# Kernel optimization log

Hardware: AMD Instinct MI355X
Metric: run time of the kernel (lower is better)

Reference implementation:

```python
import jax, jax.numpy as jnp
import numpy as np

B, S, E, H = 4, 4096, 1024, 128

def setup_inputs() -> dict:
    key = jax.random.key(0)
    kx, kk, kq, kv = jax.random.split(key, 4)
    x = jax.random.normal(kx, (B, S, E), dtype=jnp.float32)
    # torch nn.Linear weights are [out_features, in_features]
    Wk = jax.random.normal(kk, (H, E), dtype=jnp.float32) * (E ** -0.5)
    Wq = jax.random.normal(kq, (H, E), dtype=jnp.float32) * (E ** -0.5)
    Wv = jax.random.normal(kv, (H, E), dtype=jnp.float32) * (E ** -0.5)
    return {"x": x, "Wk": Wk, "Wq": Wq, "Wv": Wv}

def reference(x, Wk, Wq, Wv):
    # projections: y = x @ W.T  (bias-free nn.Linear)
    k = jnp.einsum('bse,he->bsh', x, Wk)
    q = jnp.einsum('bse,he->bsh', x, Wq)
    v = jnp.einsum('bse,he->bsh', x, Wv)
    emb = x.shape[-1]
    # scores scaled by embedding_size**-0.5 (as in the source, not head_size)
    scores = jnp.einsum('bqh,bkh->bqk', q, k) * (emb ** -0.5)  # [B,S,S]
    # causal mask: positions j > i get -inf
    i = jnp.arange(scores.shape[-2])[:, None]
    j = jnp.arange(scores.shape[-1])[None, :]
    scores = jnp.where(j > i, jnp.float32(-jnp.inf), scores)
    probs = jax.nn.softmax(scores, axis=-1)
    # dropout is identity in eval mode
    out = jnp.einsum('bqk,bkh->bqh', probs, v)  # [B,S,H]
    return out
```

## Files before the change

kernel.cpp:

```cpp
#include <hip/hip_runtime.h>

typedef short bf16x8 __attribute__((ext_vector_type(8)));
typedef float f32x4 __attribute__((ext_vector_type(4)));

#define MFMA16(a, b, c) __builtin_amdgcn_mfma_f32_16x16x32_bf16(a, b, c, 0, 0, 0)

constexpr int Bn = 4, Sn = 4096, En = 1024, Hn = 128;
constexpr float CSCALE = 1.44269504089f * 0.03125f;

__device__ inline int sbase(int qt2) {
    int a = qt2 >> 3, r = qt2 & 7;
    return (a + 1) * (4 * a + r);
}
constexpr int SLOT2_F = 16640;
constexpr int NIT = 320;

__device__ inline unsigned short f2bf(float f) {
    unsigned int u = __builtin_bit_cast(unsigned int, f);
    u += 0x7fff + ((u >> 16) & 1);
    return (unsigned short)(u >> 16);
}

__device__ inline unsigned int pk2(float a, float b) {
    unsigned int ua = __builtin_bit_cast(unsigned int, a) + 0x8000u;
    unsigned int ub = __builtin_bit_cast(unsigned int, b) + 0x8000u;
    return __builtin_amdgcn_perm(ub, ua, 0x07060302u);
}

__device__ inline void gld16(const unsigned short* g, unsigned short* l) {
    __builtin_amdgcn_global_load_lds((const __attribute__((address_space(1))) void*)g,
                                     (__attribute__((address_space(3))) void*)l, 16, 0, 0);
}

__global__ __launch_bounds__(256) void prep_kernel(
    const float* __restrict__ Wk, const float* __restrict__ Wq, const float* __restrict__ Wv,
    unsigned short* __restrict__ wb, unsigned int* __restrict__ sched)
{
    int gy = blockIdx.x >> 5;
    const float* src = (gy == 0) ? Wq : (gy == 1) ? Wk : Wv;
    unsigned short* dst = wb + (size_t)gy * Hn * En;
    int t = (blockIdx.x & 31) * 256 + threadIdx.x;
    const float4* s4 = (const float4*)src;
    for (int i = 0; i < 4; ++i) {
        float4 v = s4[(size_t)t * 4 + i];
        uint2 w2 = { pk2(v.x, v.y), pk2(v.z, v.w) };
        *(uint2*)&dst[(size_t)t * 16 + i * 4] = w2;
    }
    if (blockIdx.x == 0 && threadIdx.x < 80) {
        const int p = threadIdx.x;
        int qt2 = 0, ch = 0, acc = 0;
        for (int q = 0; q < 32; ++q) {
            int n = (q >> 3) + 1;
            if (p < acc + n) { qt2 = q; ch = p - acc; break; }
            acc += n;
        }
        int nloc = min(16, 2 * qt2 + 2 - 16 * ch);
        int key = nloc * 64 + qt2;
        int rank = 0;
        for (int p2 = 0; p2 < 80; ++p2) {
            int q2 = 0, c2 = 0, a2 = 0;
            for (int q = 0; q < 32; ++q) {
                int n = (q >> 3) + 1;
                if (p2 < a2 + n) { q2 = q; c2 = p2 - a2; break; }
                a2 += n;
            }
            int nl2 = min(16, 2 * q2 + 2 - 16 * c2);
            int k2 = nl2 * 64 + q2;
            if (k2 > key || (k2 == key && p2 < p)) ++rank;
        }
        for (int b = 0; b < 4; ++b)
            sched[rank * 4 + b] = (unsigned int)(qt2 | (ch << 6) | (b << 8));
    }
}

__global__ __launch_bounds__(256, 3) void proj_kernel(
    const float* __restrict__ x, const unsigned short* __restrict__ wb,
    unsigned short* __restrict__ qb, unsigned short* __restrict__ kb,
    unsigned short* __restrict__ vbT)
{
    __shared__ __align__(16) unsigned short xs[2][64][64];
    __shared__ __align__(16) unsigned short wsm[2][128][64];

    const int gy = blockIdx.y;
    const unsigned short* wg = wb + (size_t)gy * Hn * En;

    const int m0 = blockIdx.x * 64;
    const int tid = threadIdx.x;
    const int lane = tid & 63, wave = tid >> 6;
    const int l15 = lane & 15, quad = lane >> 4;
    const int wm = (wave & 1) * 32;
    const int wn = (wave >> 1) * 64;

    f32x4 acc[2][4] = {};
    float4 xp[4];

    auto loadx = [&](int kc) {
        for (int p4 = 0; p4 < 4; ++p4) {
            int i = p4 * 256 + tid, row = i >> 4, c4 = (i & 15) * 4;
            xp[p4] = *(const float4*)&x[(size_t)(m0 + row) * En + kc * 64 + c4];
        }
    };
    auto writex = [&](int c) {
        for (int p4 = 0; p4 < 4; ++p4) {
            int i = p4 * 256 + tid, row = i >> 4, hc = i & 15;
            uint2 w2 = { pk2(xp[p4].x, xp[p4].y), pk2(xp[p4].z, xp[p4].w) };
            *(uint2*)((char*)&xs[c][0][0] + row * 128 + (((hc >> 1) ^ (row & 7)) << 4) + ((hc & 1) << 3)) = w2;
        }
    };
    auto issueW = [&](int kc, int c) {
        for (int j = 0; j < 4; ++j) {
            int seg = (wave * 4 + j) * 1024;
            int d = seg + (lane << 4);
            int row = d >> 7, chp = (d >> 4) & 7;
            gld16(wg + (size_t)row * En + kc * 64 + ((chp ^ (row & 7)) << 3),
                  (unsigned short*)((char*)&wsm[c][0][0] + seg));
        }
    };

    loadx(0);
    issueW(0, 0);
    writex(0);
    loadx(1);

    for (int kc = 0; kc < En / 64; ++kc) {
        const int c = kc & 1;
        __syncthreads();
        if (kc + 1 < En / 64) {
            issueW(kc + 1, c ^ 1);
            writex(c ^ 1);
            int kn = (kc + 2 < En / 64) ? kc + 2 : En / 64 - 1;
            loadx(kn);
        }
        bf16x8 xf[2][2], wf[4][2];
        for (int i = 0; i < 2; ++i)
            for (int kk = 0; kk < 2; ++kk) {
                int row = wm + i * 16 + l15;
                int chn = (kk * 4 + quad) ^ (row & 7);
                xf[i][kk] = *(const bf16x8*)((char*)&xs[c][0][0] + row * 128 + (chn << 4));
            }
        for (int j = 0; j < 4; ++j)
            for (int kk = 0; kk < 2; ++kk) {
                int row = wn + j * 16 + l15;
                int chn = (kk * 4 + quad) ^ (row & 7);
                wf[j][kk] = *(const bf16x8*)((char*)&wsm[c][0][0] + row * 128 + (chn << 4));
            }
        if (gy != 2) {
            for (int kk = 0; kk < 2; ++kk)
                for (int i = 0; i < 2; ++i)
                    for (int j = 0; j < 4; ++j)
                        acc[i][j] = MFMA16(xf[i][kk], wf[j][kk], acc[i][j]);
        } else {
            for (int kk = 0; kk < 2; ++kk)
                for (int i = 0; i < 2; ++i)
                    for (int j = 0; j < 4; ++j)
                        acc[i][j] = MFMA16(wf[j][kk], xf[i][kk], acc[i][j]);
        }
    }

    if (gy != 2) {
        unsigned short* ob = (gy == 0) ? qb : kb;
        const float osc = (gy == 0) ? CSCALE : 1.0f;
        for (int i = 0; i < 2; ++i) {
            int rowb = m0 + wm + i * 16 + quad * 4;
            for (int j = 0; j < 4; ++j) {
                int col = wn + j * 16 + l15;
                for (int r = 0; r < 4; ++r)
                    ob[(size_t)(rowb + r) * Hn + col] = f2bf(acc[i][j][r] * osc);
            }
        }
    } else {
        for (int j = 0; j < 4; ++j) {
            int hb = wn + j * 16 + quad * 4;
            for (int i = 0; i < 2; ++i) {
                int sp = m0 + wm + i * 16 + l15;
                int bb = sp >> 12, ss = sp & 4095;
                for (int r = 0; r < 4; ++r)
                    vbT[((size_t)(bb * 128 + hb + r)) * Sn + ss] = f2bf(acc[i][j][r]);
            }
        }
    }
}

__global__ __launch_bounds__(256, 2) void attn_kernel(
    const unsigned short* __restrict__ qb, const unsigned short* __restrict__ kb,
    const unsigned short* __restrict__ vbT, float* __restrict__ out,
    float* __restrict__ part, const unsigned int* __restrict__ sched)
{
    __shared__ unsigned short ks[64][132];
    __shared__ unsigned short vt[128][68];
    __shared__ unsigned short ps[4][32][72];

    const unsigned int wi = sched[blockIdx.x];
    const int qt2 = (int)(wi & 63u);
    const int ch  = (int)((wi >> 6) & 3u);
    const int b   = (int)((wi >> 8) & 3u);
    const int T2  = 2 * qt2 + 2;
    const int nch = (qt2 >> 3) + 1;
    const int t0 = ch * 16;
    const int nloc = min(16, T2 - t0);
    const int q0 = qt2 * 128;

    const int tid = threadIdx.x;
    const int lane = tid & 63, wave = tid >> 6;
    const int l15 = lane & 15, quad = lane >> 4;

    const unsigned short* qg = qb + (size_t)(b * Sn + q0) * Hn;
    bf16x8 qf[2][4];
    for (int g = 0; g < 2; ++g)
        for (int f = 0; f < 4; ++f)
            qf[g][f] = *(const bf16x8*)&qg[(wave * 32 + g * 16 + l15) * Hn + f * 32 + quad * 8];

    f32x4 o[2][8] = {};
    float m_r[2] = { -INFINITY, -INFINITY }, l_r[2] = { 0.f, 0.f };

    const unsigned short* kg = kb + (size_t)b * Sn * Hn;
    const unsigned short* vg = vbT + (size_t)b * 128 * Sn;

    bf16x8 kreg[4], vreg[4];
    auto loadKV = [&](int gt) {
        int kt0 = gt * 64;
        for (int p4 = 0; p4 < 4; ++p4) {
            int i = p4 * 256 + tid;
            kreg[p4] = *(const bf16x8*)&kg[(size_t)(kt0 + (i >> 4)) * Hn + (i & 15) * 8];
            vreg[p4] = *(const bf16x8*)&vg[(size_t)(i >> 3) * Sn + kt0 + (i & 7) * 8];
        }
    };

    loadKV(t0);
    for (int tl = 0; tl < nloc; ++tl) {
        const int gt = t0 + tl;
        for (int p4 = 0; p4 < 4; ++p4) {
            int i = p4 * 256 + tid;
            *(bf16x8*)&ks[i >> 4][(i & 15) * 8] = kreg[p4];
            *(bf16x8*)&vt[i >> 3][(i & 7) * 8] = vreg[p4];
        }
        __syncthreads();
        if (tl + 1 < nloc) loadKV(gt + 1);

        float u[2][4][4];
        for (int nt = 0; nt < 4; ++nt) {
            f32x4 s0 = {}, s1 = {};
            for (int kk = 0; kk < 4; ++kk) {
                bf16x8 kf = *(const bf16x8*)&ks[nt * 16 + l15][kk * 32 + quad * 8];
                s0 = MFMA16(kf, qf[0][kk], s0);
                s1 = MFMA16(kf, qf[1][kk], s1);
            }
            for (int r = 0; r < 4; ++r) { u[0][nt][r] = s0[r]; u[1][nt][r] = s1[r]; }
        }
        if (gt >= 2 * qt2) {
            int kof = (gt - 2 * qt2) * 64;
            for (int g = 0; g < 2; ++g) {
                int qq = wave * 32 + g * 16 + l15;
                for (int nt = 0; nt < 4; ++nt)
                    for (int r = 0; r < 4; ++r)
                        if (kof + nt * 16 + quad * 4 + r > qq) u[g][nt][r] = -INFINITY;
            }
        }
        for (int g = 0; g < 2; ++g) {
            float mx = -INFINITY;
            for (int nt = 0; nt < 4; ++nt)
                for (int r = 0; r < 4; ++r) mx = fmaxf(mx, u[g][nt][r]);
            mx = fmaxf(mx, __shfl_xor(mx, 16));
            mx = fmaxf(mx, __shfl_xor(mx, 32));
            float mn = fmaxf(m_r[g], mx);
            float alpha = exp2f(m_r[g] - mn);
            m_r[g] = mn;
            float sum = 0.f;
            for (int nt = 0; nt < 4; ++nt)
                for (int r = 0; r < 4; ++r) {
                    float pv = exp2f(u[g][nt][r] - mn);
                    u[g][nt][r] = pv;
                    sum += pv;
                }
            sum += __shfl_xor(sum, 16);
            sum += __shfl_xor(sum, 32);
            l_r[g] = l_r[g] * alpha + sum;

            unsigned short* psrow = &ps[wave][g * 16 + l15][0];
            for (int nt = 0; nt < 4; ++nt) {
                uint2 w2 = { pk2(u[g][nt][0], u[g][nt][1]), pk2(u[g][nt][2], u[g][nt][3]) };
                *(uint2*)&psrow[nt * 16 + quad * 4] = w2;
            }
            for (int t = 0; t < 8; ++t) o[g][t] *= alpha;
        }

        for (int k2 = 0; k2 < 2; ++k2) {
            bf16x8 pf0 = *(const bf16x8*)&ps[wave][0 * 16 + l15][k2 * 32 + quad * 8];
            bf16x8 pf1 = *(const bf16x8*)&ps[wave][1 * 16 + l15][k2 * 32 + quad * 8];
            for (int t = 0; t < 8; ++t) {
                bf16x8 vf = *(const bf16x8*)&vt[t * 16 + l15][k2 * 32 + quad * 8];
                o[0][t] = MFMA16(vf, pf0, o[0][t]);
                o[1][t] = MFMA16(vf, pf1, o[1][t]);
            }
        }
        __syncthreads();
    }

    if (nch == 1) {
        for (int g = 0; g < 2; ++g) {
            float inv = 1.0f / l_r[g];
            float* og = out + (size_t)(b * Sn + q0 + wave * 32 + g * 16 + l15) * Hn;
            for (int t = 0; t < 8; ++t) {
                float4 st = { o[g][t][0] * inv, o[g][t][1] * inv, o[g][t][2] * inv, o[g][t][3] * inv };
                *(float4*)&og[t * 16 + quad * 4] = st;
            }
        }
    } else {
        float* P = part + (size_t)(b * 80 + sbase(qt2) + ch) * SLOT2_F;
        for (int g = 0; g < 2; ++g) {
            int q = wave * 32 + g * 16 + l15;
            for (int t = 0; t < 8; ++t) {
                float4 st = { o[g][t][0], o[g][t][1], o[g][t][2], o[g][t][3] };
                *(float4*)&P[q * 128 + t * 16 + quad * 4] = st;
            }
            if (quad == 0) {
                P[16384 + q] = m_r[g];
                P[16512 + q] = l_r[g];
            }
        }
    }
}

__global__ __launch_bounds__(256) void merge_kernel(
    const float* __restrict__ part, float* __restrict__ out)
{
    const int qt2 = 8 + (blockIdx.x >> 1);
    const int half = blockIdx.x & 1;
    const int b = blockIdx.y;
    const int nch = (qt2 >> 3) + 1;
    const float* P0 = part + (size_t)(b * 80 + sbase(qt2)) * SLOT2_F;
    const int q = half * 64 + (threadIdx.x >> 2);
    const int h0 = (threadIdx.x & 3) * 32;

    float m[4], w[4];
    float M = -INFINITY;
    for (int c = 0; c < nch; ++c) {
        m[c] = P0[(size_t)c * SLOT2_F + 16384 + q];
        M = fmaxf(M, m[c]);
    }
    float L = 0.f;
    for (int c = 0; c < nch; ++c) {
        w[c] = exp2f(m[c] - M);
        L += w[c] * P0[(size_t)c * SLOT2_F + 16512 + q];
    }
    float inv = 1.0f / L;

    float acc[32] = {};
    for (int c = 0; c < nch; ++c) {
        const float* Pq = P0 + (size_t)c * SLOT2_F + q * 128 + h0;
        for (int j = 0; j < 8; ++j) {
            float4 v = *(const float4*)&Pq[j * 4];
            acc[j * 4 + 0] += w[c] * v.x;
            acc[j * 4 + 1] += w[c] * v.y;
            acc[j * 4 + 2] += w[c] * v.z;
            acc[j * 4 + 3] += w[c] * v.w;
        }
    }
    float* og = out + (size_t)(b * Sn + qt2 * 128 + q) * Hn + h0;
    for (int j = 0; j < 8; ++j) {
        float4 st = { acc[j * 4 + 0] * inv, acc[j * 4 + 1] * inv,
                      acc[j * 4 + 2] * inv, acc[j * 4 + 3] * inv };
        *(float4*)&og[j * 4] = st;
    }
}

extern "C" void kernel_launch(void* const* d_in, const int* in_sizes, int n_in,
                              void* d_out, int out_size, void* d_ws, size_t ws_size,
                              hipStream_t stream)
{
    const float* x  = (const float*)d_in[0];
    const float* Wk = (const float*)d_in[1];
    const float* Wq = (const float*)d_in[2];
    const float* Wv = (const float*)d_in[3];
    float* out = (float*)d_out;

    unsigned short* qbuf  = (unsigned short*)d_ws;
    unsigned short* kbuf  = qbuf + (size_t)Bn * Sn * Hn;
    unsigned short* vbufT = kbuf + (size_t)Bn * Sn * Hn;
    unsigned short* wb    = vbufT + (size_t)Bn * Sn * Hn;
    float* part = (float*)(wb + (size_t)3 * Hn * En);
    unsigned int* sched = (unsigned int*)part;

    prep_kernel<<<96, 256, 0, stream>>>(Wk, Wq, Wv, wb, sched);
    proj_kernel<<<dim3(Bn * Sn / 64, 3), 256, 0, stream>>>(x, wb, qbuf, kbuf, vbufT);
    attn_kernel<<<NIT, 256, 0, stream>>>(qbuf, kbuf, vbufT, out, part, sched);
    merge_kernel<<<dim3(48, Bn), 256, 0, stream>>>(part, out);
}
```

Measured before the change: 186.8 us.

## Fuse QKV projection into one block, split attention finer, read K/V directly

The projection kernel now computes Q, K and V together in 512-thread blocks, so each x tile is read and converted once instead of three times. V is written transposed with packed 8-byte stores. Attention work is split into 8-tile chunks, and a new schedule places 768 items into 256-slot bins, with empty slots exiting early. The attention kernel drops its LDS staging and barriers for K/V and loads MFMA fragments straight from global memory, relying on cache reuse across waves. This raises occupancy but risks uncoalesced global fragment loads and more partial results to merge.

New measurement: 236.7 us. 1.27x slower.

```diff
diff --git a/kernel.cpp b/kernel.cpp
--- a/kernel.cpp
+++ b/kernel.cpp
@@ -8,12 +8,12 @@
 constexpr int Bn = 4, Sn = 4096, En = 1024, Hn = 128;
 constexpr float CSCALE = 1.44269504089f * 0.03125f;
 
-__device__ inline int sbase(int qt2) {
-    int a = qt2 >> 3, r = qt2 & 7;
-    return (a + 1) * (4 * a + r);
-}
+__device__ inline int sbase2(int qt2) {
+    int g = (qt2 - 4) >> 2, r = (qt2 - 4) & 3;
+    return 2 * g * g + 6 * g + r * (g + 2);
+}
+constexpr int NSLOT = 140;
 constexpr int SLOT2_F = 16640;
-constexpr int NIT = 320;
 
 __device__ inline unsigned short f2bf(float f) {
     unsigned int u = __builtin_bit_cast(unsigned int, f);
@@ -46,73 +46,79 @@
         uint2 w2 = { pk2(v.x, v.y), pk2(v.z, v.w) };
         *(uint2*)&dst[(size_t)t * 16 + i * 4] = w2;
     }
-    if (blockIdx.x == 0 && threadIdx.x < 80) {
-        const int p = threadIdx.x;
-        int qt2 = 0, ch = 0, acc = 0;
-        for (int q = 0; q < 32; ++q) {
-            int n = (q >> 3) + 1;
-            if (p < acc + n) { qt2 = q; ch = p - acc; break; }
-            acc += n;
-        }
-        int nloc = min(16, 2 * qt2 + 2 - 16 * ch);
-        int key = nloc * 64 + qt2;
-        int rank = 0;
-        for (int p2 = 0; p2 < 80; ++p2) {
-            int q2 = 0, c2 = 0, a2 = 0;
-            for (int q = 0; q < 32; ++q) {
-                int n = (q >> 3) + 1;
-                if (p2 < a2 + n) { q2 = q; c2 = p2 - a2; break; }
-                a2 += n;
-            }
-            int nl2 = min(16, 2 * q2 + 2 - 16 * c2);
-            int k2 = nl2 * 64 + q2;
-            if (k2 > key || (k2 == key && p2 < p)) ++rank;
-        }
-        for (int b = 0; b < 4; ++b)
-            sched[rank * 4 + b] = (unsigned int)(qt2 | (ch << 6) | (b << 8));
-    }
-}
-
-__global__ __launch_bounds__(256, 3) void proj_kernel(
+    if (blockIdx.x == 0) {
+        const int bin = threadIdx.x;
+        unsigned int it[3] = { 0xFFFFu, 0xFFFFu, 0xFFFFu };
+        auto fullItem = [](int F) -> unsigned int {
+            int b = F / 120, j = F % 120;
+            int qt2 = 31, ch = 0;
+            for (int q = 31; q >= 0; --q) {
+                int nf = (q + 1) >> 2;
+                if (j < nf) { qt2 = q; ch = j; break; }
+                j -= nf;
+            }
+            return (unsigned int)(qt2 | (ch << 5) | (b << 8));
+        };
+        auto remItem = [](int v, int t) -> unsigned int {
+            int b = t >> 3, i = t & 7;
+            int qt2 = 4 * i + (v >> 1) - 1;
+            int ch = (qt2 + 1) >> 2;
+            return (unsigned int)(qt2 | (ch << 5) | (b << 8));
+        };
+        if (bin < 192) {
+            it[0] = fullItem(2 * bin);
+            it[1] = fullItem(2 * bin + 1);
+        } else if (bin < 224) {
+            int t2 = bin - 192;
+            it[0] = fullItem(384 + 2 * t2);
+            it[1] = fullItem(385 + 2 * t2);
+            it[2] = remItem(2, t2);
+        } else {
+            int t2 = bin - 224;
+            it[0] = fullItem(448 + t2);
+            it[1] = remItem(6, t2);
+            it[2] = remItem(4, t2);
+        }
+        for (int z = 0; z < 3; ++z) sched[z * 256 + bin] = it[z];
+    }
+}
+
+__global__ __launch_bounds__(512, 2) void proj_kernel(
     const float* __restrict__ x, const unsigned short* __restrict__ wb,
     unsigned short* __restrict__ qb, unsigned short* __restrict__ kb,
     unsigned short* __restrict__ vbT)
 {
     __shared__ __align__(16) unsigned short xs[2][64][64];
-    __shared__ __align__(16) unsigned short wsm[2][128][64];
-
-    const int gy = blockIdx.y;
-    const unsigned short* wg = wb + (size_t)gy * Hn * En;
+    __shared__ __align__(16) unsigned short wsm[2][384][64];
 
     const int m0 = blockIdx.x * 64;
     const int tid = threadIdx.x;
     const int lane = tid & 63, wave = tid >> 6;
     const int l15 = lane & 15, quad = lane >> 4;
-    const int wm = (wave & 1) * 32;
-    const int wn = (wave >> 1) * 64;
-
-    f32x4 acc[2][4] = {};
-    float4 xp[4];
+    const int wn = wave * 48;
+
+    f32x4 acc[4][3] = {};
+    float4 xp[2];
 
     auto loadx = [&](int kc) {
-        for (int p4 = 0; p4 < 4; ++p4) {
-            int i = p4 * 256 + tid, row = i >> 4, c4 = (i & 15) * 4;
-            xp[p4] = *(const float4*)&x[(size_t)(m0 + row) * En + kc * 64 + c4];
+        for (int p2 = 0; p2 < 2; ++p2) {
+            int i = p2 * 512 + tid, row = i >> 4, c4 = (i & 15) * 4;
+            xp[p2] = *(const float4*)&x[(size_t)(m0 + row) * En + kc * 64 + c4];
         }
     };
     auto writex = [&](int c) {
-        for (int p4 = 0; p4 < 4; ++p4) {
-            int i = p4 * 256 + tid, row = i >> 4, hc = i & 15;
-            uint2 w2 = { pk2(xp[p4].x, xp[p4].y), pk2(xp[p4].z, xp[p4].w) };
+        for (int p2 = 0; p2 < 2; ++p2) {
+            int i = p2 * 512 + tid, row = i >> 4, hc = i & 15;
+            uint2 w2 = { pk2(xp[p2].x, xp[p2].y), pk2(xp[p2].z, xp[p2].w) };
             *(uint2*)((char*)&xs[c][0][0] + row * 128 + (((hc >> 1) ^ (row & 7)) << 4) + ((hc & 1) << 3)) = w2;
         }
     };
     auto issueW = [&](int kc, int c) {
-        for (int j = 0; j < 4; ++j) {
-            int seg = (wave * 4 + j) * 1024;
+        for (int j = 0; j < 6; ++j) {
+            int seg = (wave * 6 + j) * 1024;
             int d = seg + (lane << 4);
             int row = d >> 7, chp = (d >> 4) & 7;
-            gld16(wg + (size_t)row * En + kc * 64 + ((chp ^ (row & 7)) << 3),
+            gld16(wb + (size_t)row * En + kc * 64 + ((chp ^ (row & 7)) << 3),
                   (unsigned short*)((char*)&wsm[c][0][0] + seg));
         }
     };
@@ -131,73 +137,61 @@
             int kn = (kc + 2 < En / 64) ? kc + 2 : En / 64 - 1;
             loadx(kn);
         }
-        bf16x8 xf[2][2], wf[4][2];
-        for (int i = 0; i < 2; ++i)
+        bf16x8 xf[4][2], wf[3][2];
+        for (int i = 0; i < 4; ++i)
             for (int kk = 0; kk < 2; ++kk) {
-                int row = wm + i * 16 + l15;
+                int row = i * 16 + l15;
                 int chn = (kk * 4 + quad) ^ (row & 7);
                 xf[i][kk] = *(const bf16x8*)((char*)&xs[c][0][0] + row * 128 + (chn << 4));
             }
-        for (int j = 0; j < 4; ++j)
+        for (int j = 0; j < 3; ++j)
             for (int kk = 0; kk < 2; ++kk) {
                 int row = wn + j * 16 + l15;
                 int chn = (kk * 4 + quad) ^ (row & 7);
                 wf[j][kk] = *(const bf16x8*)((char*)&wsm[c][0][0] + row * 128 + (chn << 4));
             }
-        if (gy != 2) {
-            for (int kk = 0; kk < 2; ++kk)
-                for (int i = 0; i < 2; ++i)
-                    for (int j = 0; j < 4; ++j)
-                        acc[i][j] = MFMA16(xf[i][kk], wf[j][kk], acc[i][j]);
-        } else {
-            for (int kk = 0; kk < 2; ++kk)
-                for (int i = 0; i < 2; ++i)
-                    for (int j = 0; j < 4; ++j)
-                        acc[i][j] = MFMA16(wf[j][kk], xf[i][kk], acc[i][j]);
-        }
-    }
-
-    if (gy != 2) {
-        unsigned short* ob = (gy == 0) ? qb : kb;
-        const float osc = (gy == 0) ? CSCALE : 1.0f;
-        for (int i = 0; i < 2; ++i) {
-            int rowb = m0 + wm + i * 16 + quad * 4;
-            for (int j = 0; j < 4; ++j) {
-                int col = wn + j * 16 + l15;
+        for (int kk = 0; kk < 2; ++kk)
+            for (int i = 0; i < 4; ++i)
+                for (int j = 0; j < 3; ++j)
+                    acc[i][j] = MFMA16(xf[i][kk], wf[j][kk], acc[i][j]);
+    }
+
+    for (int i = 0; i < 4; ++i) {
+        int rowb = m0 + i * 16 + quad * 4;
+        for (int j = 0; j < 3; ++j) {
+            int gcol = wn + j * 16 + l15;
+            int gy = gcol >> 7, col = gcol & 127;
+            if (gy == 0) {
                 for (int r = 0; r < 4; ++r)
-                    ob[(size_t)(rowb + r) * Hn + col] = f2bf(acc[i][j][r] * osc);
-            }
-        }
-    } else {
-        for (int j = 0; j < 4; ++j) {
-            int hb = wn + j * 16 + quad * 4;
-            for (int i = 0; i < 2; ++i) {
-                int sp = m0 + wm + i * 16 + l15;
-                int bb = sp >> 12, ss = sp & 4095;
+                    qb[(size_t)(rowb + r) * Hn + col] = f2bf(acc[i][j][r] * CSCALE);
+            } else if (gy == 1) {
                 for (int r = 0; r < 4; ++r)
-                    vbT[((size_t)(bb * 128 + hb + r)) * Sn + ss] = f2bf(acc[i][j][r]);
-            }
-        }
-    }
-}
-
-__global__ __launch_bounds__(256, 2) void attn_kernel(
+                    kb[(size_t)(rowb + r) * Hn + col] = f2bf(acc[i][j][r]);
+            } else {
+                int bb = rowb >> 12, ss = rowb & 4095;
+                uint2 w2 = { pk2(acc[i][j][0], acc[i][j][1]), pk2(acc[i][j][2], acc[i][j][3]) };
+                *(uint2*)&vbT[((size_t)(bb * 128 + col)) * Sn + ss] = w2;
+            }
+        }
+    }
+}
+
+__global__ __launch_bounds__(256, 3) void attn_kernel(
     const unsigned short* __restrict__ qb, const unsigned short* __restrict__ kb,
     const unsigned short* __restrict__ vbT, float* __restrict__ out,
     float* __restrict__ part, const unsigned int* __restrict__ sched)
 {
-    __shared__ unsigned short ks[64][132];
-    __shared__ unsigned short vt[128][68];
     __shared__ unsigned short ps[4][32][72];
 
     const unsigned int wi = sched[blockIdx.x];
-    const int qt2 = (int)(wi & 63u);
-    const int ch  = (int)((wi >> 6) & 3u);
+    if (wi == 0xFFFFu) return;
+    const int qt2 = (int)(wi & 31u);
+    const int ch  = (int)((wi >> 5) & 7u);
     const int b   = (int)((wi >> 8) & 3u);
     const int T2  = 2 * qt2 + 2;
-    const int nch = (qt2 >> 3) + 1;
-    const int t0 = ch * 16;
-    const int nloc = min(16, T2 - t0);
+    const int nch = (qt2 + 4) >> 2;
+    const int t0 = ch * 8;
+    const int nloc = min(8, T2 - t0);
     const int q0 = qt2 * 128;
 
     const int tid = threadIdx.x;
@@ -216,32 +210,15 @@
     const unsigned short* kg = kb + (size_t)b * Sn * Hn;
     const unsigned short* vg = vbT + (size_t)b * 128 * Sn;
 
-    bf16x8 kreg[4], vreg[4];
-    auto loadKV = [&](int gt) {
-        int kt0 = gt * 64;
-        for (int p4 = 0; p4 < 4; ++p4) {
-            int i = p4 * 256 + tid;
-            kreg[p4] = *(const bf16x8*)&kg[(size_t)(kt0 + (i >> 4)) * Hn + (i & 15) * 8];
-            vreg[p4] = *(const bf16x8*)&vg[(size_t)(i >> 3) * Sn + kt0 + (i & 7) * 8];
-        }
-    };
-
-    loadKV(t0);
     for (int tl = 0; tl < nloc; ++tl) {
         const int gt = t0 + tl;
-        for (int p4 = 0; p4 < 4; ++p4) {
-            int i = p4 * 256 + tid;
-            *(bf16x8*)&ks[i >> 4][(i & 15) * 8] = kreg[p4];
-            *(bf16x8*)&vt[i >> 3][(i & 7) * 8] = vreg[p4];
-        }
-        __syncthreads();
-        if (tl + 1 < nloc) loadKV(gt + 1);
+        const int kt0 = gt * 64;
 
         float u[2][4][4];
         for (int nt = 0; nt < 4; ++nt) {
             f32x4 s0 = {}, s1 = {};
             for (int kk = 0; kk < 4; ++kk) {
-                bf16x8 kf = *(const bf16x8*)&ks[nt * 16 + l15][kk * 32 + quad * 8];
+                bf16x8 kf = *(const bf16x8*)&kg[(size_t)(kt0 + nt * 16 + l15) * Hn + kk * 32 + quad * 8];
                 s0 = MFMA16(kf, qf[0][kk], s0);
                 s1 = MFMA16(kf, qf[1][kk], s1);
             }
@@ -288,12 +265,11 @@
             bf16x8 pf0 = *(const bf16x8*)&ps[wave][0 * 16 + l15][k2 * 32 + quad * 8];
             bf16x8 pf1 = *(const bf16x8*)&ps[wave][1 * 16 + l15][k2 * 32 + quad * 8];
             for (int t = 0; t < 8; ++t) {
-                bf16x8 vf = *(const bf16x8*)&vt[t * 16 + l15][k2 * 32 + quad * 8];
+                bf16x8 vf = *(const bf16x8*)&vg[(size_t)(t * 16 + l15) * Sn + kt0 + k2 * 32 + quad * 8];
                 o[0][t] = MFMA16(vf, pf0, o[0][t]);
                 o[1][t] = MFMA16(vf, pf1, o[1][t]);
             }
         }
-        __syncthreads();
     }
 
     if (nch == 1) {
@@ -306,7 +282,7 @@
             }
         }
     } else {
-        float* P = part + (size_t)(b * 80 + sbase(qt2) + ch) * SLOT2_F;
+        float* P = part + (size_t)(b * NSLOT + sbase2(qt2) + ch) * SLOT2_F;
         for (int g = 0; g < 2; ++g) {
             int q = wave * 32 + g * 16 + l15;
             for (int t = 0; t < 8; ++t) {
@@ -324,15 +300,15 @@
 __global__ __launch_bounds__(256) void merge_kernel(
     const float* __restrict__ part, float* __restrict__ out)
 {
-    const int qt2 = 8 + (blockIdx.x >> 1);
+    const int qt2 = 4 + (blockIdx.x >> 1);
     const int half = blockIdx.x & 1;
     const int b = blockIdx.y;
-    const int nch = (qt2 >> 3) + 1;
-    const float* P0 = part + (size_t)(b * 80 + sbase(qt2)) * SLOT2_F;
+    const int nch = (qt2 + 4) >> 2;
+    const float* P0 = part + (size_t)(b * NSLOT + sbase2(qt2)) * SLOT2_F;
     const int q = half * 64 + (threadIdx.x >> 2);
     const int h0 = (threadIdx.x & 3) * 32;
 
-    float m[4], w[4];
+    float m[8], w[8];
     float M = -INFINITY;
     for (int c = 0; c < nch; ++c) {
         m[c] = P0[(size_t)c * SLOT2_F + 16384 + q];
@@ -378,11 +354,11 @@
     unsigned short* kbuf  = qbuf + (size_t)Bn * Sn * Hn;
     unsigned short* vbufT = kbuf + (size_t)Bn * Sn * Hn;
     unsigned short* wb    = vbufT + (size_t)Bn * Sn * Hn;
-    float* part = (float*)(wb + (size_t)3 * Hn * En);
-    unsigned int* sched = (unsigned int*)part;
+    unsigned int* sched   = (unsigned int*)(wb + (size_t)3 * Hn * En);
+    float* part = (float*)(sched + 1024);
 
     prep_kernel<<<96, 256, 0, stream>>>(Wk, Wq, Wv, wb, sched);
-    proj_kernel<<<dim3(Bn * Sn / 64, 3), 256, 0, stream>>>(x, wb, qbuf, kbuf, vbufT);
-    attn_kernel<<<NIT, 256, 0, stream>>>(qbuf, kbuf, vbufT, out, part, sched);
-    merge_kernel<<<dim3(48, Bn), 256, 0, stream>>>(part, out);
-}
+    proj_kernel<<<256, 512, 0, stream>>>(x, wb, qbuf, kbuf, vbufT);
+    attn_kernel<<<768, 256, 0, stream>>>(qbuf, kbuf, vbufT, out, part, sched);
+    merge_kernel<<<dim3(56, Bn), 256, 0, stream>>>(part, out);
+}
```
